# Kernel optimization log

Hardware: AMD Instinct MI355X
Metric: run time of the kernel (lower is better)

## Reference

```python
import jax, jax.numpy as jnp
import numpy as np

SEQ_LEN = 12
B = 1024
NG = 32            # scenes
G = B // NG        # pedestrians per scene
E = 64             # embedding_dim
H = 128            # h_dim
PP = 512           # mlp_pre_pool hidden
BOT = 1024         # bottleneck_dim
MLPD = 1024        # mlp_dim


def _w(key, fan_in, shape):
    return jax.random.normal(key, shape, jnp.float32) / np.sqrt(fan_in)


def setup_inputs():
    key = jax.random.key(0)
    ks = jax.random.split(key, 16)
    starts = jnp.arange(NG, dtype=jnp.int32) * G
    inp = {
        'last_pos': jax.random.normal(ks[0], (B, 2), jnp.float32),
        'last_pos_rel': jax.random.normal(ks[1], (B, 2), jnp.float32) * 0.1,
        'decoder_h': jax.random.normal(ks[2], (1, B, H), jnp.float32) * 0.1,
        'decoder_c': jax.random.normal(ks[3], (1, B, H), jnp.float32) * 0.1,
        'seq_start_end': jnp.stack([starts, starts + G], axis=1),
        'W_emb': _w(ks[4], 2, (2, E)), 'b_emb': jnp.zeros((E,), jnp.float32),
        'W_ih': _w(ks[5], E, (4 * H, E)), 'b_ih': jnp.zeros((4 * H,), jnp.float32),
        'W_hh': _w(ks[6], H, (4 * H, H)), 'b_hh': jnp.zeros((4 * H,), jnp.float32),
        'W_h2p': _w(ks[7], H, (H, 2)), 'b_h2p': jnp.zeros((2,), jnp.float32),
        'W_sp': _w(ks[8], 2, (2, E)), 'b_sp': jnp.zeros((E,), jnp.float32),
        'W_pp1': _w(ks[9], E + H, (E + H, PP)), 'b_pp1': jnp.zeros((PP,), jnp.float32),
        'W_pp2': _w(ks[10], PP, (PP, BOT)), 'b_pp2': jnp.zeros((BOT,), jnp.float32),
        'W_m1': _w(ks[11], H + BOT, (H + BOT, MLPD)), 'b_m1': jnp.zeros((MLPD,), jnp.float32),
        'W_m2': _w(ks[12], MLPD, (MLPD, H)), 'b_m2': jnp.zeros((H,), jnp.float32),
    }
    return inp


def _forward(last_pos, last_pos_rel, h0, c0,
             W_emb, b_emb, W_ih, b_ih, W_hh, b_hh, W_h2p, b_h2p,
             W_sp, b_sp, W_pp1, b_pp1, W_pp2, b_pp2, W_m1, b_m1, W_m2, b_m2):
    relu = jax.nn.relu

    def pool_net(h, pos):
        # PoolHiddenNet over NG contiguous equal-size groups of G peds.
        hg = h.reshape(NG, G, H)
        pg = pos.reshape(NG, G, 2)
        # rel[g, i, j] = pos_j - pos_i  (matches repeat/tile ordering in torch code)
        rel = pg[:, None, :, :] - pg[:, :, None, :]          # [NG,G,G,2]
        emb = rel @ W_sp + b_sp                               # [NG,G,G,E]
        hj = jnp.broadcast_to(hg[:, None, :, :], (NG, G, G, H))
        x = jnp.concatenate([emb, hj], axis=-1)               # [NG,G,G,E+H]
        x = relu(x @ W_pp1 + b_pp1)
        x = relu(x @ W_pp2 + b_pp2)                           # [NG,G,G,BOT]
        return jnp.max(x, axis=2).reshape(B, BOT)             # max over neighbors j

    def lstm_cell(x, h, c):
        gates = x @ W_ih.T + b_ih + h @ W_hh.T + b_hh
        i, f, g, o = jnp.split(gates, 4, axis=-1)
        c2 = jax.nn.sigmoid(f) * c + jax.nn.sigmoid(i) * jnp.tanh(g)
        h2 = jax.nn.sigmoid(o) * jnp.tanh(c2)
        return h2, c2

    dec_in0 = last_pos_rel @ W_emb + b_emb

    def step(carry, _):
        lp, din, h, c = carry
        h, c = lstm_cell(din, h, c)
        rel_pos = h @ W_h2p + b_h2p                           # [B,2]
        curr_pos = rel_pos + lp
        pool_h = pool_net(h, curr_pos)                        # [B,BOT]
        hcat = jnp.concatenate([h, pool_h], axis=1)
        h = relu(relu(hcat @ W_m1 + b_m1) @ W_m2 + b_m2)      # refreshed decoder_h
        din = rel_pos @ W_emb + b_emb
        return (curr_pos, din, h, c), rel_pos

    (_, _, h_fin, _), pred = jax.lax.scan(
        step, (last_pos, dec_in0, h0, c0), None, length=SEQ_LEN)
    return pred, h_fin[None]                                  # [T,B,2], [1,B,H]


def reference(last_pos, last_pos_rel, decoder_h, decoder_c, seq_start_end,
              W_emb, b_emb, W_ih, b_ih, W_hh, b_hh, W_h2p, b_h2p,
              W_sp, b_sp, W_pp1, b_pp1, W_pp2, b_pp2, W_m1, b_m1, W_m2, b_m2):
    del seq_start_end  # uniform contiguous groups encoded statically (NG, G)
    return _forward(last_pos, last_pos_rel, decoder_h[0], decoder_c[0],
                    W_emb, b_emb, W_ih, b_ih, W_hh, b_hh, W_h2p, b_h2p,
                    W_sp, b_sp, W_pp1, b_pp1, W_pp2, b_pp2, W_m1, b_m1, W_m2, b_m2)
```

## Files before the change

kernel.cpp:

```cpp
#include <hip/hip_runtime.h>
#include <math.h>

#define T_SEQ 12

typedef __bf16 bf16x8 __attribute__((ext_vector_type(8)));
typedef float f32x4 __attribute__((ext_vector_type(4)));
typedef unsigned short u16x8 __attribute__((ext_vector_type(8)));

static __device__ __forceinline__ unsigned short bf16bits(float x) {
  return __builtin_bit_cast(unsigned short, (__bf16)x);
}
static __device__ __forceinline__ bf16x8 asbf(u16x8 v) {
  return __builtin_bit_cast(bf16x8, v);
}

enum : int {
  OFF_LP    = 0,
  OFF_DIN   = 2048,
  OFF_C     = 198656,
  OFF_HDEC  = 329728,
  OFF_WC    = 460800,
  OFF_BC    = 461824,
  OFF_PW    = 462336,
  OFF_AA    = 986624,
  OFF_WP2T  = 1510912,
  OFF_WM1T  = 1773056,
  OFF_HCATB = 2362880,
  OFF_WM2TB = 2952704,
  OFF_MIDB  = 3018240,
  OFF_WIHT  = 3542528,
  OFF_WHHT  = 3575296,
  OFF_WFRAG = 3640832
};

#define SWZP(byte, row) ((byte) ^ (((row) & 7) << 4))

__global__ __launch_bounds__(256) void k_setup(
    const float* __restrict__ last_pos, const float* __restrict__ lpr,
    const float* __restrict__ dh, const float* __restrict__ dc,
    const float* __restrict__ W_emb, const float* __restrict__ b_emb,
    float* __restrict__ lp, float* __restrict__ din,
    float* __restrict__ h_dec, float* __restrict__ c) {
  int idx = blockIdx.x * 256 + threadIdx.x;
  if (idx < 2048) lp[idx] = last_pos[idx];
  h_dec[idx] = dh[idx];
  c[idx] = dc[idx];
  if (idx < 65536) {
    int b = idx >> 6, e = idx & 63;
    din[idx] = lpr[b*2] * W_emb[e] + lpr[b*2+1] * W_emb[64+e] + b_emb[e];
  }
}

__global__ __launch_bounds__(256) void k_wc(
    const float* __restrict__ W_sp, const float* __restrict__ b_sp,
    const float* __restrict__ W_pp1, const float* __restrict__ b_pp1,
    float* __restrict__ Wc, float* __restrict__ bc) {
  int n = blockIdx.x * 256 + threadIdx.x;
  if (n >= 512) return;
  float a0 = 0.f, a1 = 0.f, ab = 0.f;
#pragma unroll 8
  for (int k = 0; k < 64; k++) {
    float w = W_pp1[k*512 + n];
    a0 += W_sp[k] * w;
    a1 += W_sp[64+k] * w;
    ab += b_sp[k] * w;
  }
  Wc[n] = a0; Wc[512+n] = a1; bc[n] = ab + b_pp1[n];
}

__global__ __launch_bounds__(256) void k_tcvt(
    const float* __restrict__ src, unsigned short* __restrict__ dst,
    int R, int C) {
  __shared__ float t[32][33];
  const int bx = blockIdx.x * 32, by = blockIdx.y * 32;
  const int tx = threadIdx.x & 31, ty = threadIdx.x >> 5;
#pragma unroll
  for (int i = 0; i < 32; i += 8) t[ty+i][tx] = src[(size_t)(by+ty+i)*C + bx+tx];
  __syncthreads();
#pragma unroll
  for (int i = 0; i < 32; i += 8)
    dst[(size_t)(bx+ty+i)*R + by+tx] = bf16bits(t[tx][ty+i]);
}

__global__ __launch_bounds__(256) void k_t32(
    const float* __restrict__ src, float* __restrict__ dst, int R, int C) {
  __shared__ float t[32][33];
  const int bx = blockIdx.x * 32, by = blockIdx.y * 32;
  const int tx = threadIdx.x & 31, ty = threadIdx.x >> 5;
#pragma unroll
  for (int i = 0; i < 32; i += 8) t[ty+i][tx] = src[(size_t)(by+ty+i)*C + bx+tx];
  __syncthreads();
#pragma unroll
  for (int i = 0; i < 32; i += 8)
    dst[(size_t)(bx+ty+i)*R + by+tx] = t[tx][ty+i];
}

__global__ __launch_bounds__(256) void k_frag(
    const unsigned short* __restrict__ Wp2t, unsigned short* __restrict__ Wfrag) {
  const int tid = blockIdx.x * 256 + threadIdx.x;
  const int fid = tid >> 6, l = tid & 63;
  const int nbb = fid >> 4, ks = fid & 15;
  u16x8 v = *(const u16x8*)(Wp2t + (size_t)(nbb*16 + (l & 15))*512 +
                            ks*32 + (l >> 4)*8);
  *(u16x8*)(Wfrag + (size_t)tid*8) = v;
}

__global__ __launch_bounds__(512) void k_step1(
    float* __restrict__ din, const float* __restrict__ h_dec,
    float* __restrict__ cst, unsigned short* __restrict__ hcatB,
    float* __restrict__ lp, float* __restrict__ pred,
    const float* __restrict__ Wiht, const float* __restrict__ b_ih,
    const float* __restrict__ Whht, const float* __restrict__ b_hh,
    const float* __restrict__ W_h2p, const float* __restrict__ b_h2p,
    const float* __restrict__ W_emb, const float* __restrict__ b_emb,
    const float* __restrict__ W1b, const float* __restrict__ Wc,
    const float* __restrict__ bc,
    float* __restrict__ PW, float* __restrict__ Aa, int t) {
  const int b0 = blockIdx.x * 4;
  const int tid = threadIdx.x;
  __shared__ float xh[4*192];
  __shared__ float gl[4*512];
  __shared__ float hbuf[4*128];
  __shared__ float relS[8], curS[8];

  for (int i = tid; i < 768; i += 512) {
    int r = i / 192, k = i - r*192;
    xh[i] = (k < 64) ? din[(b0+r)*64 + k] : h_dec[(b0+r)*128 + k - 64];
  }
  __syncthreads();
  {
    const int n = tid;
    float bias = b_ih[n] + b_hh[n];
    float acc[4] = {bias, bias, bias, bias};
#pragma unroll 8
    for (int k = 0; k < 64; k++) {
      float wv = Wiht[k*512 + n];
#pragma unroll
      for (int r = 0; r < 4; r++) acc[r] += xh[r*192 + k] * wv;
    }
#pragma unroll 8
    for (int k = 0; k < 128; k++) {
      float wv = Whht[k*512 + n];
#pragma unroll
      for (int r = 0; r < 4; r++) acc[r] += xh[r*192 + 64 + k] * wv;
    }
#pragma unroll
    for (int r = 0; r < 4; r++) gl[r*512 + n] = acc[r];
  }
  __syncthreads();
  {
    int r = tid >> 7, hh = tid & 127;
    float ig = gl[r*512 + hh],       fg = gl[r*512 + 128 + hh];
    float gg = gl[r*512 + 256 + hh], og = gl[r*512 + 384 + hh];
    ig = 1.f/(1.f+expf(-ig)); fg = 1.f/(1.f+expf(-fg));
    gg = tanhf(gg);           og = 1.f/(1.f+expf(-og));
    int row = b0 + r;
    float c2 = fg * cst[row*128 + hh] + ig * gg;
    float h2 = og * tanhf(c2);
    cst[row*128 + hh] = c2;
    hbuf[r*128 + hh] = h2;
    hcatB[(size_t)row*1152 + hh] = bf16bits(h2);
  }
  __syncthreads();
  if (tid < 128) {
    int r = tid >> 5, col = (tid >> 4) & 1, l16 = tid & 15;
    float s = 0.f;
    for (int k = l16; k < 128; k += 16) s += hbuf[r*128 + k] * W_h2p[k*2 + col];
#pragma unroll
    for (int off = 8; off > 0; off >>= 1) s += __shfl_xor(s, off);
    if (l16 == 0) {
      float rel = s + b_h2p[col];
      float old = lp[(b0+r)*2 + col];
      relS[r*2 + col] = rel;
      curS[r*2 + col] = old + rel;
      lp[(b0+r)*2 + col] = old + rel;
      pred[t*2048 + (b0+r)*2 + col] = rel;
    }
  }
  __syncthreads();
  if (tid < 256) {
    int r = tid >> 6, e = tid & 63;
    din[(b0+r)*64 + e] = relS[r*2]*W_emb[e] + relS[r*2+1]*W_emb[64+e] + b_emb[e];
  }
  {
    const int n = tid;
    float acc[4] = {0.f, 0.f, 0.f, 0.f};
#pragma unroll 4
    for (int k = 0; k < 128; k++) {
      float wv = W1b[k*512 + n];
#pragma unroll
      for (int r = 0; r < 4; r++) acc[r] += hbuf[r*128 + k] * wv;
    }
    float wc0 = Wc[n], wc1 = Wc[512+n], bcv = bc[n];
#pragma unroll
    for (int r = 0; r < 4; r++) {
      float pw = curS[r*2]*wc0 + curS[r*2+1]*wc1;
      PW[(size_t)(b0+r)*512 + n] = pw;
      Aa[(size_t)(b0+r)*512 + n] = acc[r] + pw + bcv;
    }
  }
}

__global__ __launch_bounds__(512) void k_pool8(
    const float* __restrict__ Aa, const float* __restrict__ PW,
    const unsigned short* __restrict__ Wfrag, const float* __restrict__ bp2,
    unsigned short* __restrict__ hcatB) {
  const int bid = blockIdx.x;
  const int mt = (bid >> 3) & 7;
  const int g  = (bid & 7) + ((bid >> 6) << 3);
  const int tid = threadIdx.x, lane = tid & 63, w = tid >> 6;
  const int wr = w >> 2, wc = w & 3;
  const int l15 = lane & 15, lhi = lane >> 4;
  __shared__ __align__(128) char lds[163840];
  char* As = lds;
  char* B0 = lds + 131072;
  char* B1 = lds + 131072 + 16384;

  {
    const int ke = lane * 8;
#pragma unroll 4
    for (int rr = 0; rr < 16; rr++) {
      const int r = rr * 8 + w;
      const int j = r & 31, ii = r >> 5;
      const float* aRow = Aa + (size_t)(g*32 + j)*512 + ke;
      const float* pRow = PW + (size_t)(g*32 + mt*4 + ii)*512 + ke;
      float4 a0 = *(const float4*)aRow;
      float4 a1 = *(const float4*)(aRow + 4);
      float4 p0 = *(const float4*)pRow;
      float4 p1 = *(const float4*)(pRow + 4);
      bf16x8 y;
      y[0] = (__bf16)fmaxf(a0.x - p0.x, 0.f);
      y[1] = (__bf16)fmaxf(a0.y - p0.y, 0.f);
      y[2] = (__bf16)fmaxf(a0.z - p0.z, 0.f);
      y[3] = (__bf16)fmaxf(a0.w - p0.w, 0.f);
      y[4] = (__bf16)fmaxf(a1.x - p1.x, 0.f);
      y[5] = (__bf16)fmaxf(a1.y - p1.y, 0.f);
      y[6] = (__bf16)fmaxf(a1.z - p1.z, 0.f);
      y[7] = (__bf16)fmaxf(a1.w - p1.w, 0.f);
      *(bf16x8*)(As + SWZP(r*1024 + lane*16, r)) = y;
    }
  }

  const int u0 = tid, u1 = tid + 512;
  const size_t gfo0 = (size_t)((u0 >> 6) * 16) * 512 + (u0 & 63) * 8;
  const size_t gfo1 = (size_t)((u1 >> 6) * 16) * 512 + (u1 & 63) * 8;

  {
    u16x8 s0 = *(const u16x8*)(Wfrag + gfo0);
    u16x8 s1 = *(const u16x8*)(Wfrag + gfo1);
    *(u16x8*)(B0 + u0*16) = s0;
    *(u16x8*)(B0 + u1*16) = s1;
  }
  u16x8 r0, r1;
  {
    const size_t base = (size_t)1 * 512;
    r0 = *(const u16x8*)(Wfrag + base + gfo0);
    r1 = *(const u16x8*)(Wfrag + base + gfo1);
  }
  __syncthreads();

  for (int nt = 0; nt < 4; nt++) {
    f32x4 acc[4][4] = {};
    for (int k0 = 0; k0 < 16; k0++) {
      const int q = nt*16 + k0;
      char* Bcur = (q & 1) ? B1 : B0;
      char* Bnxt = (q & 1) ? B0 : B1;
      if (q < 63) {
        *(u16x8*)(Bnxt + u0*16) = r0;
        *(u16x8*)(Bnxt + u1*16) = r1;
      }
      if (q < 62) {
        const int q2 = q + 2;
        const size_t base = (size_t)((q2 >> 4) * 256 + (q2 & 15)) * 512;
        r0 = *(const u16x8*)(Wfrag + base + gfo0);
        r1 = *(const u16x8*)(Wfrag + base + gfo1);
      }
      bf16x8 af[4], bfr[4];
#pragma unroll
      for (int mf = 0; mf < 4; mf++) {
        const int row = wr*64 + mf*16 + l15;
        af[mf] = *(const bf16x8*)(As + SWZP(row*1024 + k0*64 + lhi*16, row));
      }
#pragma unroll
      for (int nf = 0; nf < 4; nf++)
        bfr[nf] = *(const bf16x8*)(Bcur + (wc*4 + nf)*1024 + lane*16);
#pragma unroll
      for (int mf = 0; mf < 4; mf++)
#pragma unroll
        for (int nf = 0; nf < 4; nf++)
          acc[mf][nf] = __builtin_amdgcn_mfma_f32_16x16x32_bf16(
              af[mf], bfr[nf], acc[mf][nf], 0, 0, 0);
      __syncthreads();
    }
#pragma unroll
    for (int isub = 0; isub < 2; isub++)
#pragma unroll
      for (int nf = 0; nf < 4; nf++) {
        f32x4 v0 = acc[isub*2][nf], v1 = acc[isub*2 + 1][nf];
        float mx = fmaxf(fmaxf(fmaxf(v0[0], v0[1]), fmaxf(v0[2], v0[3])),
                         fmaxf(fmaxf(v1[0], v1[1]), fmaxf(v1[2], v1[3])));
        mx = fmaxf(mx, __shfl_xor(mx, 16));
        mx = fmaxf(mx, __shfl_xor(mx, 32));
        if (lane < 16) {
          const int n = nt*256 + wc*64 + nf*16 + lane;
          const int i = mt*4 + wr*2 + isub;
          hcatB[(size_t)(g*32 + i)*1152 + 128 + n] =
              bf16bits(fmaxf(mx + bp2[n], 0.f));
        }
      }
  }
}

__global__ __launch_bounds__(256) void k_m1s(
    const unsigned short* __restrict__ A, const unsigned short* __restrict__ Bw,
    const float* __restrict__ bias, unsigned short* __restrict__ outB) {
  const int nt = blockIdx.x, mt = blockIdx.y;
  const int tid = threadIdx.x, lane = tid & 63, w = tid >> 6;
  const int wr = w >> 1, wc = w & 1;
  const int l15 = lane & 15, lhi = lane >> 4;
  __shared__ __align__(128) char lds[16384];

  const int srow = tid >> 3, sslot = tid & 7;
  const unsigned short* aSrc = A  + (size_t)(mt*64)*1152;
  const unsigned short* bSrc = Bw + (size_t)(nt*64)*1152;

  u16x8 cur0, cur1, cur2, cur3;
  cur0 = *(const u16x8*)(aSrc + (size_t)srow*1152      + sslot*8);
  cur1 = *(const u16x8*)(aSrc + (size_t)(32+srow)*1152 + sslot*8);
  cur2 = *(const u16x8*)(bSrc + (size_t)srow*1152      + sslot*8);
  cur3 = *(const u16x8*)(bSrc + (size_t)(32+srow)*1152 + sslot*8);
  *(u16x8*)(lds + SWZP(srow*128 + sslot*16, srow)) = cur0;
  *(u16x8*)(lds + SWZP((32+srow)*128 + sslot*16, 32+srow)) = cur1;
  *(u16x8*)(lds + 8192 + SWZP(srow*128 + sslot*16, srow)) = cur2;
  *(u16x8*)(lds + 8192 + SWZP((32+srow)*128 + sslot*16, 32+srow)) = cur3;
  __syncthreads();

  f32x4 acc[2][2] = {};
  for (int c = 0; c < 18; c++) {
    u16x8 nx0, nx1, nx2, nx3;
    if (c < 17) {
      const int kb = (c+1)*64 + sslot*8;
      nx0 = *(const u16x8*)(aSrc + (size_t)srow*1152      + kb);
      nx1 = *(const u16x8*)(aSrc + (size_t)(32+srow)*1152 + kb);
      nx2 = *(const u16x8*)(bSrc + (size_t)srow*1152      + kb);
      nx3 = *(const u16x8*)(bSrc + (size_t)(32+srow)*1152 + kb);
    }
    bf16x8 af[2][2], bf_[2][2];
#pragma unroll
    for (int ks = 0; ks < 2; ks++) {
#pragma unroll
      for (int mf = 0; mf < 2; mf++) {
        const int row = wr*32 + mf*16 + l15;
        af[mf][ks] = *(const bf16x8*)(lds + SWZP(row*128 + ks*64 + lhi*16, row));
      }
#pragma unroll
      for (int nf = 0; nf < 2; nf++) {
        const int row = wc*32 + nf*16 + l15;
        bf_[nf][ks] = *(const bf16x8*)(lds + 8192 + SWZP(row*128 + ks*64 + lhi*16, row));
      }
    }
#pragma unroll
    for (int ks = 0; ks < 2; ks++)
#pragma unroll
      for (int mf = 0; mf < 2; mf++)
#pragma unroll
        for (int nf = 0; nf < 2; nf++)
          acc[mf][nf] = __builtin_amdgcn_mfma_f32_16x16x32_bf16(
              af[mf][ks], bf_[nf][ks], acc[mf][nf], 0, 0, 0);
    __syncthreads();
    if (c < 17) {
      *(u16x8*)(lds + SWZP(srow*128 + sslot*16, srow)) = nx0;
      *(u16x8*)(lds + SWZP((32+srow)*128 + sslot*16, 32+srow)) = nx1;
      *(u16x8*)(lds + 8192 + SWZP(srow*128 + sslot*16, srow)) = nx2;
      *(u16x8*)(lds + 8192 + SWZP((32+srow)*128 + sslot*16, 32+srow)) = nx3;
      __syncthreads();
    }
  }
#pragma unroll
  for (int mf = 0; mf < 2; mf++)
#pragma unroll
    for (int nf = 0; nf < 2; nf++) {
      const int col = nt*64 + wc*32 + nf*16 + l15;
      const float bv = bias[col];
#pragma unroll
      for (int r = 0; r < 4; r++) {
        const int row = mt*64 + wr*32 + mf*16 + lhi*4 + r;
        outB[(size_t)row*1024 + col] = bf16bits(fmaxf(acc[mf][nf][r] + bv, 0.f));
      }
    }
}

__global__ __launch_bounds__(256) void k_m2s(
    const unsigned short* __restrict__ A, const unsigned short* __restrict__ Bw,
    const float* __restrict__ bias, float* __restrict__ hd) {
  const int nt = blockIdx.x, mt = blockIdx.y;
  const int tid = threadIdx.x, lane = tid & 63, w = tid >> 6;
  const int wr = w >> 1, wc = w & 1;
  const int l15 = lane & 15, lhi = lane >> 4;
  __shared__ __align__(128) char lds[16384];

  const int srow = tid >> 3, sslot = tid & 7;
  const unsigned short* aSrc = A  + (size_t)(mt*64)*1024;
  const unsigned short* bSrc = Bw + (size_t)(nt*64)*1024;

  u16x8 cur0, cur1, cur2, cur3;
  cur0 = *(const u16x8*)(aSrc + (size_t)srow*1024      + sslot*8);
  cur1 = *(const u16x8*)(aSrc + (size_t)(32+srow)*1024 + sslot*8);
  cur2 = *(const u16x8*)(bSrc + (size_t)srow*1024      + sslot*8);
  cur3 = *(const u16x8*)(bSrc + (size_t)(32+srow)*1024 + sslot*8);
  *(u16x8*)(lds + SWZP(srow*128 + sslot*16, srow)) = cur0;
  *(u16x8*)(lds + SWZP((32+srow)*128 + sslot*16, 32+srow)) = cur1;
  *(u16x8*)(lds + 8192 + SWZP(srow*128 + sslot*16, srow)) = cur2;
  *(u16x8*)(lds + 8192 + SWZP((32+srow)*128 + sslot*16, 32+srow)) = cur3;
  __syncthreads();

  f32x4 acc[2][2] = {};
  for (int c = 0; c < 16; c++) {
    u16x8 nx0, nx1, nx2, nx3;
    if (c < 15) {
      const int kb = (c+1)*64 + sslot*8;
      nx0 = *(const u16x8*)(aSrc + (size_t)srow*1024      + kb);
      nx1 = *(const u16x8*)(aSrc + (size_t)(32+srow)*1024 + kb);
      nx2 = *(const u16x8*)(bSrc + (size_t)srow*1024      + kb);
      nx3 = *(const u16x8*)(bSrc + (size_t)(32+srow)*1024 + kb);
    }
    bf16x8 af[2][2], bf_[2][2];
#pragma unroll
    for (int ks = 0; ks < 2; ks++) {
#pragma unroll
      for (int mf = 0; mf < 2; mf++) {
        const int row = wr*32 + mf*16 + l15;
        af[mf][ks] = *(const bf16x8*)(lds + SWZP(row*128 + ks*64 + lhi*16, row));
      }
#pragma unroll
      for (int nf = 0; nf < 2; nf++) {
        const int row = wc*32 + nf*16 + l15;
        bf_[nf][ks] = *(const bf16x8*)(lds + 8192 + SWZP(row*128 + ks*64 + lhi*16, row));
      }
    }
#pragma unroll
    for (int ks = 0; ks < 2; ks++)
#pragma unroll
      for (int mf = 0; mf < 2; mf++)
#pragma unroll
        for (int nf = 0; nf < 2; nf++)
          acc[mf][nf] = __builtin_amdgcn_mfma_f32_16x16x32_bf16(
              af[mf][ks], bf_[nf][ks], acc[mf][nf], 0, 0, 0);
    __syncthreads();
    if (c < 15) {
      *(u16x8*)(lds + SWZP(srow*128 + sslot*16, srow)) = nx0;
      *(u16x8*)(lds + SWZP((32+srow)*128 + sslot*16, 32+srow)) = nx1;
      *(u16x8*)(lds + 8192 + SWZP(srow*128 + sslot*16, srow)) = nx2;
      *(u16x8*)(lds + 8192 + SWZP((32+srow)*128 + sslot*16, 32+srow)) = nx3;
      __syncthreads();
    }
  }
#pragma unroll
  for (int mf = 0; mf < 2; mf++)
#pragma unroll
    for (int nf = 0; nf < 2; nf++) {
      const int col = nt*64 + wc*32 + nf*16 + l15;
      const float bv = bias[col];
#pragma unroll
      for (int r = 0; r < 4; r++) {
        const int row = mt*64 + wr*32 + mf*16 + lhi*4 + r;
        hd[(size_t)row*128 + col] = fmaxf(acc[mf][nf][r] + bv, 0.f);
      }
    }
}

__global__ __launch_bounds__(256) void k_hfin(const float* __restrict__ h_dec,
                                              float* __restrict__ out) {
  int idx = blockIdx.x * 256 + threadIdx.x;
  if (idx < 131072) out[24576 + idx] = h_dec[idx];
}

extern "C" void kernel_launch(void* const* d_in, const int* in_sizes, int n_in,
                              void* d_out, int out_size, void* d_ws, size_t ws_size,
                              hipStream_t stream) {
  const float* last_pos = (const float*)d_in[0];
  const float* lpr      = (const float*)d_in[1];
  const float* dh       = (const float*)d_in[2];
  const float* dc       = (const float*)d_in[3];
  const float* W_emb = (const float*)d_in[5];
  const float* b_emb = (const float*)d_in[6];
  const float* W_ih  = (const float*)d_in[7];
  const float* b_ih  = (const float*)d_in[8];
  const float* W_hh  = (const float*)d_in[9];
  const float* b_hh  = (const float*)d_in[10];
  const float* W_h2p = (const float*)d_in[11];
  const float* b_h2p = (const float*)d_in[12];
  const float* W_sp  = (const float*)d_in[13];
  const float* b_sp  = (const float*)d_in[14];
  const float* W_pp1 = (const float*)d_in[15];
  const float* b_pp1 = (const float*)d_in[16];
  const float* W_pp2 = (const float*)d_in[17];
  const float* b_pp2 = (const float*)d_in[18];
  const float* W_m1  = (const float*)d_in[19];
  const float* b_m1  = (const float*)d_in[20];
  const float* W_m2  = (const float*)d_in[21];
  const float* b_m2  = (const float*)d_in[22];

  float* ws    = (float*)d_ws;
  float* lp    = ws + OFF_LP;
  float* din   = ws + OFF_DIN;
  float* cst   = ws + OFF_C;
  float* h_dec = ws + OFF_HDEC;
  float* Wc    = ws + OFF_WC;
  float* bc    = ws + OFF_BC;
  float* PW    = ws + OFF_PW;
  float* Aa    = ws + OFF_AA;
  unsigned short* Wp2t  = (unsigned short*)(ws + OFF_WP2T);
  unsigned short* Wm1t  = (unsigned short*)(ws + OFF_WM1T);
  unsigned short* hcatB = (unsigned short*)(ws + OFF_HCATB);
  unsigned short* Wm2tB = (unsigned short*)(ws + OFF_WM2TB);
  unsigned short* midB  = (unsigned short*)(ws + OFF_MIDB);
  float* Wiht  = ws + OFF_WIHT;
  float* Whht  = ws + OFF_WHHT;
  unsigned short* Wfrag = (unsigned short*)(ws + OFF_WFRAG);
  float* out   = (float*)d_out;

  k_setup<<<512, 256, 0, stream>>>(last_pos, lpr, dh, dc, W_emb, b_emb, lp, din, h_dec, cst);
  k_wc<<<2, 256, 0, stream>>>(W_sp, b_sp, W_pp1, b_pp1, Wc, bc);
  { dim3 gt(32, 16); k_tcvt<<<gt, 256, 0, stream>>>(W_pp2, Wp2t, 512, 1024); }
  { dim3 gt(32, 36); k_tcvt<<<gt, 256, 0, stream>>>(W_m1, Wm1t, 1152, 1024); }
  { dim3 gt(4, 32);  k_tcvt<<<gt, 256, 0, stream>>>(W_m2, Wm2tB, 1024, 128); }
  { dim3 gt(2, 16);  k_t32<<<gt, 256, 0, stream>>>(W_ih, Wiht, 512, 64); }
  { dim3 gt(4, 16);  k_t32<<<gt, 256, 0, stream>>>(W_hh, Whht, 512, 128); }
  k_frag<<<256, 256, 0, stream>>>(Wp2t, Wfrag);

  for (int t = 0; t < T_SEQ; t++) {
    k_step1<<<256, 512, 0, stream>>>(din, h_dec, cst, hcatB, lp, out,
                                     Wiht, b_ih, Whht, b_hh, W_h2p, b_h2p,
                                     W_emb, b_emb, W_pp1 + 64*512, Wc, bc,
                                     PW, Aa, t);
    k_pool8<<<256, 512, 0, stream>>>(Aa, PW, Wfrag, b_pp2, hcatB);
    { dim3 gm(16, 16); k_m1s<<<gm, 256, 0, stream>>>(hcatB, Wm1t, b_m1, midB); }
    { dim3 gm(2, 16);  k_m2s<<<gm, 256, 0, stream>>>(midB, Wm2tB, b_m2, h_dec); }
  }
  k_hfin<<<512, 256, 0, stream>>>(h_dec, out);
}
```

Measured before the change: 1.049 ms.

## Rewrite MLP GEMMs with intra-block split-K, wider K chunks and LDS reduction

The two per-step MLP GEMM kernels now split the K dimension across the four waves instead of splitting the output tile. Each block stages K chunks of 128 in double-buffered LDS and reduces the partial accumulators through LDS before the bias+ReLU epilogue. The second GEMM halves its M tile to 32 to launch twice as many blocks, and the pool kernel's inner loop gets an unroll pragma. This aims to cut barrier count and per-chunk load latency for these small-N GEMMs, at the cost of much larger LDS footprints (64KB/48KB), lower occupancy, and an extra reduction pass.

```diff
diff --git a/kernel.cpp b/kernel.cpp
--- a/kernel.cpp
+++ b/kernel.cpp
@@ -9,9 +9,6 @@
 
 static __device__ __forceinline__ unsigned short bf16bits(float x) {
   return __builtin_bit_cast(unsigned short, (__bf16)x);
-}
-static __device__ __forceinline__ bf16x8 asbf(u16x8 v) {
-  return __builtin_bit_cast(bf16x8, v);
 }
 
 enum : int {
@@ -253,7 +250,7 @@
   }
   u16x8 r0, r1;
   {
-    const size_t base = (size_t)1 * 512;
+    const size_t base = (size_t)512;
     r0 = *(const u16x8*)(Wfrag + base + gfo0);
     r1 = *(const u16x8*)(Wfrag + base + gfo1);
   }
@@ -261,6 +258,7 @@
 
   for (int nt = 0; nt < 4; nt++) {
     f32x4 acc[4][4] = {};
+#pragma unroll 4
     for (int k0 = 0; k0 < 16; k0++) {
       const int q = nt*16 + k0;
       char* Bcur = (q & 1) ? B1 : B0;
@@ -311,162 +309,202 @@
   }
 }
 
-__global__ __launch_bounds__(256) void k_m1s(
+__global__ __launch_bounds__(256) void k_m1k(
     const unsigned short* __restrict__ A, const unsigned short* __restrict__ Bw,
     const float* __restrict__ bias, unsigned short* __restrict__ outB) {
   const int nt = blockIdx.x, mt = blockIdx.y;
   const int tid = threadIdx.x, lane = tid & 63, w = tid >> 6;
-  const int wr = w >> 1, wc = w & 1;
   const int l15 = lane & 15, lhi = lane >> 4;
-  __shared__ __align__(128) char lds[16384];
-
-  const int srow = tid >> 3, sslot = tid & 7;
+  __shared__ __align__(128) char lds[65536];
   const unsigned short* aSrc = A  + (size_t)(mt*64)*1152;
   const unsigned short* bSrc = Bw + (size_t)(nt*64)*1152;
 
-  u16x8 cur0, cur1, cur2, cur3;
-  cur0 = *(const u16x8*)(aSrc + (size_t)srow*1152      + sslot*8);
-  cur1 = *(const u16x8*)(aSrc + (size_t)(32+srow)*1152 + sslot*8);
-  cur2 = *(const u16x8*)(bSrc + (size_t)srow*1152      + sslot*8);
-  cur3 = *(const u16x8*)(bSrc + (size_t)(32+srow)*1152 + sslot*8);
-  *(u16x8*)(lds + SWZP(srow*128 + sslot*16, srow)) = cur0;
-  *(u16x8*)(lds + SWZP((32+srow)*128 + sslot*16, 32+srow)) = cur1;
-  *(u16x8*)(lds + 8192 + SWZP(srow*128 + sslot*16, srow)) = cur2;
-  *(u16x8*)(lds + 8192 + SWZP((32+srow)*128 + sslot*16, 32+srow)) = cur3;
-  __syncthreads();
-
-  f32x4 acc[2][2] = {};
-  for (int c = 0; c < 18; c++) {
-    u16x8 nx0, nx1, nx2, nx3;
-    if (c < 17) {
-      const int kb = (c+1)*64 + sslot*8;
-      nx0 = *(const u16x8*)(aSrc + (size_t)srow*1152      + kb);
-      nx1 = *(const u16x8*)(aSrc + (size_t)(32+srow)*1152 + kb);
-      nx2 = *(const u16x8*)(bSrc + (size_t)srow*1152      + kb);
-      nx3 = *(const u16x8*)(bSrc + (size_t)(32+srow)*1152 + kb);
-    }
-    bf16x8 af[2][2], bf_[2][2];
-#pragma unroll
-    for (int ks = 0; ks < 2; ks++) {
-#pragma unroll
-      for (int mf = 0; mf < 2; mf++) {
-        const int row = wr*32 + mf*16 + l15;
-        af[mf][ks] = *(const bf16x8*)(lds + SWZP(row*128 + ks*64 + lhi*16, row));
-      }
-#pragma unroll
-      for (int nf = 0; nf < 2; nf++) {
-        const int row = wc*32 + nf*16 + l15;
-        bf_[nf][ks] = *(const bf16x8*)(lds + 8192 + SWZP(row*128 + ks*64 + lhi*16, row));
-      }
-    }
-#pragma unroll
-    for (int ks = 0; ks < 2; ks++)
-#pragma unroll
-      for (int mf = 0; mf < 2; mf++)
-#pragma unroll
-        for (int nf = 0; nf < 2; nf++)
-          acc[mf][nf] = __builtin_amdgcn_mfma_f32_16x16x32_bf16(
-              af[mf][ks], bf_[nf][ks], acc[mf][nf], 0, 0, 0);
+  u16x8 rg[8];
+#pragma unroll
+  for (int p = 0; p < 8; p++) {
+    const int u = tid + p*256;
+    const int isB = u >> 10, v = u & 1023;
+    const int row = v >> 4, slot = v & 15;
+    u16x8 val = *(const u16x8*)((isB ? bSrc : aSrc) + (size_t)row*1152 + slot*8);
+    *(u16x8*)(lds + isB*16384 + SWZP(row*256 + slot*16, row)) = val;
+  }
+#pragma unroll
+  for (int p = 0; p < 8; p++) {
+    const int u = tid + p*256;
+    const int isB = u >> 10, v = u & 1023;
+    const int row = v >> 4, slot = v & 15;
+    rg[p] = *(const u16x8*)((isB ? bSrc : aSrc) + (size_t)row*1152 + 128 + slot*8);
+  }
+  __syncthreads();
+
+  f32x4 acc[4][4] = {};
+  for (int c = 0; c < 9; c++) {
+    const int cur = (c & 1) * 32768;
+    const int nxt = 32768 - cur;
+    if (c < 8) {
+#pragma unroll
+      for (int p = 0; p < 8; p++) {
+        const int u = tid + p*256;
+        const int isB = u >> 10, v = u & 1023;
+        const int row = v >> 4, slot = v & 15;
+        *(u16x8*)(lds + nxt + isB*16384 + SWZP(row*256 + slot*16, row)) = rg[p];
+      }
+    }
+    if (c < 7) {
+#pragma unroll
+      for (int p = 0; p < 8; p++) {
+        const int u = tid + p*256;
+        const int isB = u >> 10, v = u & 1023;
+        const int row = v >> 4, slot = v & 15;
+        rg[p] = *(const u16x8*)((isB ? bSrc : aSrc) + (size_t)row*1152 +
+                                (c+2)*128 + slot*8);
+      }
+    }
+    bf16x8 af[4], bf[4];
+#pragma unroll
+    for (int mf = 0; mf < 4; mf++) {
+      const int row = mf*16 + l15;
+      af[mf] = *(const bf16x8*)(lds + cur + SWZP(row*256 + w*64 + lhi*16, row));
+    }
+#pragma unroll
+    for (int nf = 0; nf < 4; nf++) {
+      const int row = nf*16 + l15;
+      bf[nf] = *(const bf16x8*)(lds + cur + 16384 +
+                                SWZP(row*256 + w*64 + lhi*16, row));
+    }
+#pragma unroll
+    for (int mf = 0; mf < 4; mf++)
+#pragma unroll
+      for (int nf = 0; nf < 4; nf++)
+        acc[mf][nf] = __builtin_amdgcn_mfma_f32_16x16x32_bf16(
+            af[mf], bf[nf], acc[mf][nf], 0, 0, 0);
     __syncthreads();
-    if (c < 17) {
-      *(u16x8*)(lds + SWZP(srow*128 + sslot*16, srow)) = nx0;
-      *(u16x8*)(lds + SWZP((32+srow)*128 + sslot*16, 32+srow)) = nx1;
-      *(u16x8*)(lds + 8192 + SWZP(srow*128 + sslot*16, srow)) = nx2;
-      *(u16x8*)(lds + 8192 + SWZP((32+srow)*128 + sslot*16, 32+srow)) = nx3;
-      __syncthreads();
-    }
-  }
-#pragma unroll
-  for (int mf = 0; mf < 2; mf++)
-#pragma unroll
-    for (int nf = 0; nf < 2; nf++) {
-      const int col = nt*64 + wc*32 + nf*16 + l15;
-      const float bv = bias[col];
-#pragma unroll
-      for (int r = 0; r < 4; r++) {
-        const int row = mt*64 + wr*32 + mf*16 + lhi*4 + r;
-        outB[(size_t)row*1024 + col] = bf16bits(fmaxf(acc[mf][nf][r] + bv, 0.f));
-      }
-    }
-}
-
-__global__ __launch_bounds__(256) void k_m2s(
+  }
+
+#pragma unroll
+  for (int mf = 0; mf < 4; mf++)
+#pragma unroll
+    for (int nf = 0; nf < 4; nf++)
+      *(f32x4*)(lds + w*16384 + (mf*4 + nf)*1024 + lane*16) = acc[mf][nf];
+  __syncthreads();
+#pragma unroll
+  for (int pi = 0; pi < 4; pi++) {
+    const int p = w*4 + pi;
+    f32x4 s = *(const f32x4*)(lds + p*1024 + lane*16);
+#pragma unroll
+    for (int wv = 1; wv < 4; wv++) {
+      f32x4 q = *(const f32x4*)(lds + wv*16384 + p*1024 + lane*16);
+      s[0] += q[0]; s[1] += q[1]; s[2] += q[2]; s[3] += q[3];
+    }
+    const int col = nt*64 + (p & 3)*16 + l15;
+    const float bv = bias[col];
+#pragma unroll
+    for (int r = 0; r < 4; r++) {
+      const int row = mt*64 + (p >> 2)*16 + lhi*4 + r;
+      outB[(size_t)row*1024 + col] = bf16bits(fmaxf(s[r] + bv, 0.f));
+    }
+  }
+}
+
+__global__ __launch_bounds__(256) void k_m2k(
     const unsigned short* __restrict__ A, const unsigned short* __restrict__ Bw,
     const float* __restrict__ bias, float* __restrict__ hd) {
   const int nt = blockIdx.x, mt = blockIdx.y;
   const int tid = threadIdx.x, lane = tid & 63, w = tid >> 6;
-  const int wr = w >> 1, wc = w & 1;
   const int l15 = lane & 15, lhi = lane >> 4;
-  __shared__ __align__(128) char lds[16384];
-
-  const int srow = tid >> 3, sslot = tid & 7;
-  const unsigned short* aSrc = A  + (size_t)(mt*64)*1024;
+  __shared__ __align__(128) char lds[49152];
+  const unsigned short* aSrc = A  + (size_t)(mt*32)*1024;
   const unsigned short* bSrc = Bw + (size_t)(nt*64)*1024;
 
-  u16x8 cur0, cur1, cur2, cur3;
-  cur0 = *(const u16x8*)(aSrc + (size_t)srow*1024      + sslot*8);
-  cur1 = *(const u16x8*)(aSrc + (size_t)(32+srow)*1024 + sslot*8);
-  cur2 = *(const u16x8*)(bSrc + (size_t)srow*1024      + sslot*8);
-  cur3 = *(const u16x8*)(bSrc + (size_t)(32+srow)*1024 + sslot*8);
-  *(u16x8*)(lds + SWZP(srow*128 + sslot*16, srow)) = cur0;
-  *(u16x8*)(lds + SWZP((32+srow)*128 + sslot*16, 32+srow)) = cur1;
-  *(u16x8*)(lds + 8192 + SWZP(srow*128 + sslot*16, srow)) = cur2;
-  *(u16x8*)(lds + 8192 + SWZP((32+srow)*128 + sslot*16, 32+srow)) = cur3;
-  __syncthreads();
-
-  f32x4 acc[2][2] = {};
-  for (int c = 0; c < 16; c++) {
-    u16x8 nx0, nx1, nx2, nx3;
-    if (c < 15) {
-      const int kb = (c+1)*64 + sslot*8;
-      nx0 = *(const u16x8*)(aSrc + (size_t)srow*1024      + kb);
-      nx1 = *(const u16x8*)(aSrc + (size_t)(32+srow)*1024 + kb);
-      nx2 = *(const u16x8*)(bSrc + (size_t)srow*1024      + kb);
-      nx3 = *(const u16x8*)(bSrc + (size_t)(32+srow)*1024 + kb);
-    }
-    bf16x8 af[2][2], bf_[2][2];
-#pragma unroll
-    for (int ks = 0; ks < 2; ks++) {
-#pragma unroll
-      for (int mf = 0; mf < 2; mf++) {
-        const int row = wr*32 + mf*16 + l15;
-        af[mf][ks] = *(const bf16x8*)(lds + SWZP(row*128 + ks*64 + lhi*16, row));
-      }
-#pragma unroll
-      for (int nf = 0; nf < 2; nf++) {
-        const int row = wc*32 + nf*16 + l15;
-        bf_[nf][ks] = *(const bf16x8*)(lds + 8192 + SWZP(row*128 + ks*64 + lhi*16, row));
-      }
-    }
-#pragma unroll
-    for (int ks = 0; ks < 2; ks++)
-#pragma unroll
-      for (int mf = 0; mf < 2; mf++)
-#pragma unroll
-        for (int nf = 0; nf < 2; nf++)
-          acc[mf][nf] = __builtin_amdgcn_mfma_f32_16x16x32_bf16(
-              af[mf][ks], bf_[nf][ks], acc[mf][nf], 0, 0, 0);
+  u16x8 rg[6];
+#pragma unroll
+  for (int p = 0; p < 6; p++) {
+    const int u = tid + p*256;
+    const int isB = (u >= 512);
+    const int v = isB ? (u - 512) : u;
+    const int row = v >> 4, slot = v & 15;
+    u16x8 val = *(const u16x8*)((isB ? bSrc : aSrc) + (size_t)row*1024 + slot*8);
+    *(u16x8*)(lds + isB*8192 + SWZP(row*256 + slot*16, row)) = val;
+  }
+#pragma unroll
+  for (int p = 0; p < 6; p++) {
+    const int u = tid + p*256;
+    const int isB = (u >= 512);
+    const int v = isB ? (u - 512) : u;
+    const int row = v >> 4, slot = v & 15;
+    rg[p] = *(const u16x8*)((isB ? bSrc : aSrc) + (size_t)row*1024 + 128 + slot*8);
+  }
+  __syncthreads();
+
+  f32x4 acc[2][4] = {};
+  for (int c = 0; c < 8; c++) {
+    const int cur = (c & 1) * 24576;
+    const int nxt = 24576 - cur;
+    if (c < 7) {
+#pragma unroll
+      for (int p = 0; p < 6; p++) {
+        const int u = tid + p*256;
+        const int isB = (u >= 512);
+        const int v = isB ? (u - 512) : u;
+        const int row = v >> 4, slot = v & 15;
+        *(u16x8*)(lds + nxt + isB*8192 + SWZP(row*256 + slot*16, row)) = rg[p];
+      }
+    }
+    if (c < 6) {
+#pragma unroll
+      for (int p = 0; p < 6; p++) {
+        const int u = tid + p*256;
+        const int isB = (u >= 512);
+        const int v = isB ? (u - 512) : u;
+        const int row = v >> 4, slot = v & 15;
+        rg[p] = *(const u16x8*)((isB ? bSrc : aSrc) + (size_t)row*1024 +
+                                (c+2)*128 + slot*8);
+      }
+    }
+    bf16x8 af[2], bf[4];
+#pragma unroll
+    for (int mf = 0; mf < 2; mf++) {
+      const int row = mf*16 + l15;
+      af[mf] = *(const bf16x8*)(lds + cur + SWZP(row*256 + w*64 + lhi*16, row));
+    }
+#pragma unroll
+    for (int nf = 0; nf < 4; nf++) {
+      const int row = nf*16 + l15;
+      bf[nf] = *(const bf16x8*)(lds + cur + 8192 +
+                                SWZP(row*256 + w*64 + lhi*16, row));
+    }
+#pragma unroll
+    for (int mf = 0; mf < 2; mf++)
+#pragma unroll
+      for (int nf = 0; nf < 4; nf++)
+        acc[mf][nf] = __builtin_amdgcn_mfma_f32_16x16x32_bf16(
+            af[mf], bf[nf], acc[mf][nf], 0, 0, 0);
     __syncthreads();
-    if (c < 15) {
-      *(u16x8*)(lds + SWZP(srow*128 + sslot*16, srow)) = nx0;
-      *(u16x8*)(lds + SWZP((32+srow)*128 + sslot*16, 32+srow)) = nx1;
-      *(u16x8*)(lds + 8192 + SWZP(srow*128 + sslot*16, srow)) = nx2;
-      *(u16x8*)(lds + 8192 + SWZP((32+srow)*128 + sslot*16, 32+srow)) = nx3;
-      __syncthreads();
-    }
-  }
+  }
+
 #pragma unroll
   for (int mf = 0; mf < 2; mf++)
 #pragma unroll
-    for (int nf = 0; nf < 2; nf++) {
-      const int col = nt*64 + wc*32 + nf*16 + l15;
-      const float bv = bias[col];
-#pragma unroll
-      for (int r = 0; r < 4; r++) {
-        const int row = mt*64 + wr*32 + mf*16 + lhi*4 + r;
-        hd[(size_t)row*128 + col] = fmaxf(acc[mf][nf][r] + bv, 0.f);
-      }
-    }
+    for (int nf = 0; nf < 4; nf++)
+      *(f32x4*)(lds + w*8192 + (mf*4 + nf)*1024 + lane*16) = acc[mf][nf];
+  __syncthreads();
+#pragma unroll
+  for (int pi = 0; pi < 2; pi++) {
+    const int p = w*2 + pi;
+    f32x4 s = *(const f32x4*)(lds + p*1024 + lane*16);
+#pragma unroll
+    for (int wv = 1; wv < 4; wv++) {
+      f32x4 q = *(const f32x4*)(lds + wv*8192 + p*1024 + lane*16);
+      s[0] += q[0]; s[1] += q[1]; s[2] += q[2]; s[3] += q[3];
+    }
+    const int col = nt*64 + (p & 3)*16 + l15;
+    const float bv = bias[col];
+#pragma unroll
+    for (int r = 0; r < 4; r++) {
+      const int row = mt*32 + (p >> 2)*16 + lhi*4 + r;
+      hd[(size_t)row*128 + col] = fmaxf(s[r] + bv, 0.f);
+    }
+  }
 }
 
 __global__ __launch_bounds__(256) void k_hfin(const float* __restrict__ h_dec,
@@ -535,8 +573,8 @@
                                      W_emb, b_emb, W_pp1 + 64*512, Wc, bc,
                                      PW, Aa, t);
     k_pool8<<<256, 512, 0, stream>>>(Aa, PW, Wfrag, b_pp2, hcatB);
-    { dim3 gm(16, 16); k_m1s<<<gm, 256, 0, stream>>>(hcatB, Wm1t, b_m1, midB); }
-    { dim3 gm(2, 16);  k_m2s<<<gm, 256, 0, stream>>>(midB, Wm2tB, b_m2, h_dec); }
+    { dim3 gm(16, 16); k_m1k<<<gm, 256, 0, stream>>>(hcatB, Wm1t, b_m1, midB); }
+    { dim3 gm(2, 32);  k_m2k<<<gm, 256, 0, stream>>>(midB, Wm2tB, b_m2, h_dec); }
   }
   k_hfin<<<512, 256, 0, stream>>>(h_dec, out);
 }
```

Result: faster. 994.9 us (-5.2%).
